# Optimization experiments

Measured on AMD Instinct MI355X. Metric: run time of the kernel, lower is better.

Reference implementation:

```python
import jax, jax.numpy as jnp
import numpy as np

X = 512; Y = 512; C = 3; NK = 15
DT = 0.2; DD = 2; SIGMA = 0.95
THETA_X = 2.0; N_EXP = 2.0
K_SIZE = 16

# mesh-grid positions, cell centers at +0.5 (matches construct_mesh_grid)
POS = (jnp.stack(jnp.meshgrid(jnp.arange(X), jnp.arange(Y), indexing='ij'), axis=-1) + 0.5).astype(jnp.float32)  # [X,Y,2]


def _dwconv(img, k):
    # img [X,Y,C'] -> depthwise 3x3 cross-correlation with 'same' zero padding (matches torch conv2d)
    z = img.transpose(2, 0, 1)[None]                      # [1,C',X,Y]
    kern = jnp.tile(k[None, None], (z.shape[1], 1, 1, 1))  # [C',1,3,3]
    out = jax.lax.conv_general_dilated(z, kern, (1, 1), 'SAME', feature_group_count=z.shape[1])
    return out[0].transpose(1, 2, 0)


def _sobel(img):
    # returns [X,Y,2,C'] with (sy, sx) stacked on axis 2, matching torch code order
    kx = jnp.array([[-1., 0., 1.], [-2., 0., 2.], [-1., 0., 1.]], jnp.float32)
    return jnp.stack([_dwconv(img, kx.T), _dwconv(img, kx)], axis=2)


def _reintegrate(grid, F):
    # Flow-Lenia reintegration tracking: 25 static roll offsets, fused accumulation
    ma = DD - SIGMA
    mu = POS[..., None] + jnp.clip(DT * F, -ma, ma)  # [X,Y,2,C]
    mu = jnp.clip(mu, SIGMA, X - SIGMA)
    clip_hi = min(1.0, 2.0 * SIGMA)
    inv_area = 1.0 / (4.0 * SIGMA ** 2)
    acc = jnp.zeros_like(grid)
    for dx in range(-DD, DD + 1):
        for dy in range(-DD, DD + 1):
            gridR = jnp.roll(grid, (dx, dy), (0, 1))
            muR = jnp.roll(mu, (dx, dy), (0, 1))
            sz = 0.5 - jnp.abs(POS[..., None] - muR) + SIGMA
            area = jnp.prod(jnp.clip(sz, 0.0, clip_hi), axis=2) * inv_area  # [X,Y,C]
            acc = acc + gridR * area
    return acc


def _forward(x, Ks, m, s, h, w_c1, c0):
    # spectral kernels: normalize, fftshift, fft2 (matches construct_kernels)
    Ksn = Ks / Ks.sum(axis=(0, 1), keepdims=True)
    fk = jnp.fft.fft2(jnp.fft.fftshift(Ksn, axes=(0, 1)), axes=(0, 1))  # [X,Y,NK] complex
    fXs = jnp.fft.fft2(x, axes=(0, 1))
    Us = jnp.fft.ifft2(fk * fXs[:, :, c0], axes=(0, 1)).real            # [X,Y,NK]
    # growth * h (note: h appears again inside w_c1, faithful to original double multiply)
    Gs = (jnp.exp(-(((Us - m) / s) ** 2) * 0.5) * 2.0 - 1.0) * h
    Hs = jnp.einsum('xyk,kc->xyc', Gs, w_c1)                             # [X,Y,C]
    grad_u = _sobel(Hs)                                                  # [X,Y,2,C]
    grad_x = _sobel(x.sum(-1, keepdims=True))                            # [X,Y,2,1]
    alpha = jnp.clip((x[:, :, None, :] / THETA_X) ** N_EXP, 0.0, 1.0)    # [X,Y,1,C]
    F = grad_u * (1.0 - alpha) - grad_x * alpha                          # [X,Y,2,C]
    return _reintegrate(x, F)


def setup_inputs() -> dict:
    key = jax.random.key(0)
    k1, k2, k3, k4, k5 = jax.random.split(key, 5)
    x = jax.random.uniform(k1, (X, Y, C), jnp.float32)
    # ring kernels per construct_kernels (non-sparse branch)
    mg = np.mgrid[-X // 2:X // 2, -Y // 2:Y // 2]
    base = np.linalg.norm(mg, axis=0).astype(np.float32)
    ks_list = []
    for i in range(NK):
        r = 0.6 + 0.04 * i
        D = base / ((K_SIZE + 15) * r)
        sig = 0.5 * (np.tanh(-(D - 1.0) * 10.0 / 2.0) + 1.0)
        bell = np.exp(-(D - 0.5) ** 2 / 0.15)
        ks_list.append(sig * bell)
    Ks = jnp.asarray(np.stack(ks_list, -1).astype(np.float32))
    m = 0.1 + 0.3 * jax.random.uniform(k2, (NK,), jnp.float32)
    s = 0.03 + 0.15 * jax.random.uniform(k3, (NK,), jnp.float32)
    h = 0.3 + 0.7 * jax.random.uniform(k4, (NK,), jnp.float32)
    c0 = jax.random.randint(k5, (NK,), 0, C, jnp.int32)
    c1 = jnp.arange(NK) % C
    w_c1 = jax.nn.one_hot(c1, C, dtype=jnp.float32) * h[:, None]
    return {"x": x, "Ks": Ks, "m": m, "s": s, "h": h, "w_c1": w_c1, "c0": c0}


def reference(x, Ks, m, s, h, w_c1, c0):
    return _forward(x, Ks, m, s, h, w_c1, c0)
```

## Files before the change

### kernel.cpp

```cpp
#include <hip/hip_runtime.h>
#include <math.h>

#define NPIX 262144
#define NKER 15
#define PI_F 3.14159265358979323846f
#define HW 264
#define HWR 264
#define CS 578
#define SK(n) ((n) + ((n) >> 3))

__device__ __forceinline__ float2 cadd(float2 a, float2 b) { return make_float2(a.x + b.x, a.y + b.y); }
__device__ __forceinline__ float2 csub(float2 a, float2 b) { return make_float2(a.x - b.x, a.y - b.y); }
__device__ __forceinline__ float2 cmul(float2 a, float2 b) {
  return make_float2(a.x * b.x - a.y * b.y, a.x * b.y + a.y * b.x);
}
__device__ __forceinline__ float2 cmulc(float2 a, float2 b) {
  return make_float2(a.x * b.x + a.y * b.y, a.y * b.x - a.x * b.y);
}

__device__ __forceinline__ void build_tw(int lane, float2* pA, float2* pB) {
  float s, c;
  sincosf(-2.0f * PI_F * (float)lane / 512.0f, &s, &c);
  float2 w1 = make_float2(c, s);
  int h = lane & ~7;
  float2 wh = make_float2(__shfl(c, h, 64), __shfl(s, h, 64));
  pA[0] = w1;
  pA[1] = cmul(w1, w1);
  pA[2] = cmul(pA[1], w1);
  pA[3] = cmul(pA[1], pA[1]);
  pA[4] = cmul(pA[3], w1);
  pA[5] = cmul(pA[3], pA[1]);
  pA[6] = cmul(pA[3], pA[2]);
  pB[0] = wh;
  pB[1] = cmul(wh, wh);
  pB[2] = cmul(pB[1], wh);
  pB[3] = cmul(pB[1], pB[1]);
  pB[4] = cmul(pB[3], wh);
  pB[5] = cmul(pB[3], pB[1]);
  pB[6] = cmul(pB[3], pB[2]);
}

template <bool INV>
__device__ __forceinline__ void dft8(float2 a[8]) {
  const float R = 0.70710678118654752f;
  float2 t0 = cadd(a[0], a[4]), u0 = csub(a[0], a[4]);
  float2 t1 = cadd(a[1], a[5]), u1 = csub(a[1], a[5]);
  float2 t2 = cadd(a[2], a[6]), u2 = csub(a[2], a[6]);
  float2 t3 = cadd(a[3], a[7]), u3 = csub(a[3], a[7]);
  u1 = INV ? make_float2(R * (u1.x - u1.y), R * (u1.x + u1.y))
           : make_float2(R * (u1.x + u1.y), R * (u1.y - u1.x));
  u2 = INV ? make_float2(-u2.y, u2.x) : make_float2(u2.y, -u2.x);
  u3 = INV ? make_float2(-R * (u3.x + u3.y), R * (u3.x - u3.y))
           : make_float2(R * (u3.y - u3.x), -R * (u3.x + u3.y));
  float2 e0 = cadd(t0, t2), f0 = csub(t0, t2);
  float2 e1 = cadd(t1, t3), f1 = csub(t1, t3);
  f1 = INV ? make_float2(-f1.y, f1.x) : make_float2(f1.y, -f1.x);
  float2 g0 = cadd(u0, u2), h0 = csub(u0, u2);
  float2 g1 = cadd(u1, u3), h1 = csub(u1, u3);
  h1 = INV ? make_float2(-h1.y, h1.x) : make_float2(h1.y, -h1.x);
  a[0] = cadd(e0, e1); a[4] = csub(e0, e1);
  a[2] = cadd(f0, f1); a[6] = csub(f0, f1);
  a[1] = cadd(g0, g1); a[5] = csub(g0, g1);
  a[3] = cadd(h0, h1); a[7] = csub(h0, h1);
}

template <bool INV>
__device__ __forceinline__ void fft512_r8(float2 a[8], float2* buf, int lane,
                                          const float2* pA, const float2* pB) {
  dft8<INV>(a);
#pragma unroll
  for (int q = 1; q < 8; ++q) a[q] = INV ? cmulc(a[q], pA[q - 1]) : cmul(a[q], pA[q - 1]);
#pragma unroll
  for (int q = 0; q < 8; ++q) buf[9 * lane + q] = a[q];
#pragma unroll
  for (int q = 0; q < 8; ++q) a[q] = buf[SK(lane + 64 * q)];
  dft8<INV>(a);
#pragma unroll
  for (int q = 1; q < 8; ++q) a[q] = INV ? cmulc(a[q], pB[q - 1]) : cmul(a[q], pB[q - 1]);
  int h = lane & ~7;
  int b2 = 9 * h + (lane - h);
#pragma unroll
  for (int q = 0; q < 8; ++q) buf[b2 + 9 * q] = a[q];
#pragma unroll
  for (int q = 0; q < 8; ++q) a[q] = buf[SK(lane + 64 * q)];
  dft8<INV>(a);
}

__device__ __forceinline__ void split_store_halfplane(float2 a[8], float2* buf, int lane,
                                                      float2* d0, float2* d1) {
#pragma unroll
  for (int q = 0; q < 8; ++q) buf[SK(lane + 64 * q)] = a[q];
#pragma unroll
  for (int q = 0; q < 4; ++q) {
    int v = lane + 64 * q;
    int mir = (512 - v) & 511;
    float2 P = a[q];
    float2 Qc = buf[SK(mir)];
    float2 Q = make_float2(Qc.x, -Qc.y);
    d0[v] = make_float2(0.5f * (P.x + Q.x), 0.5f * (P.y + Q.y));
    d1[v] = make_float2(0.5f * (P.y - Q.y), -0.5f * (P.x - Q.x));
  }
  if (lane == 0) {
    float2 P = a[4];
    d0[256] = make_float2(P.x, 0.f);
    d1[256] = make_float2(P.y, 0.f);
  }
}

__global__ __launch_bounds__(512, 4) void rows_all(
    const float* __restrict__ Ks, const float* __restrict__ x,
    float* __restrict__ partial, float* __restrict__ AkR,
    float2* __restrict__ AxH) {
  __shared__ float krow[512 * NKER];
  __shared__ float2 scr[8][CS];
  __shared__ float psum[480];
  int t = threadIdx.x, wave = t >> 6, lane = t & 63;
  float2 pA[7], pB[7];
  build_tw(lane, pA, pB);
  if (blockIdx.x < 512) {
    int b = blockIdx.x;
    int rs = (b + 256) & 511;
    const float2* src = (const float2*)Ks + (size_t)rs * 3840;
    float2* kr2 = (float2*)krow;
    for (int i = t; i < 3840; i += 512) kr2[i] = src[i];
    __syncthreads();
    if (t < 480) {
      int k = t >> 5, yg = t & 31;
      float s = 0.f;
      int base = yg * 16;
#pragma unroll
      for (int y = 0; y < 16; ++y) s += krow[(base + y) * NKER + k];
      psum[t] = s;
    }
    {
      int k1 = 2 * wave, k2 = k1 + 1;
      float2 a[8];
      bool nz = false;
#pragma unroll
      for (int q = 0; q < 8; ++q) {
        int ys = (lane + 64 * q + 256) & 511;
        float re = krow[ys * NKER + k1];
        float im = (k2 < NKER) ? krow[ys * NKER + k2] : 0.f;
        a[q] = make_float2(re, im);
        nz |= (re != 0.f) || (im != 0.f);
      }
      float* d0 = AkR + ((size_t)k1 * 512 + b) * HWR;
      float* d1 = AkR + ((size_t)k2 * 512 + b) * HWR;
      if (__any((int)nz)) {
        fft512_r8<false>(a, &scr[wave][0], lane, pA, pB);
#pragma unroll
        for (int q = 0; q < 4; ++q) {
          int v = lane + 64 * q;
          d0[v] = a[q].x; d1[v] = a[q].y;
        }
        if (lane == 0) { d0[256] = a[4].x; d1[256] = a[4].y; }
      } else {
#pragma unroll
        for (int q = 0; q < 4; ++q) {
          int v = lane + 64 * q;
          d0[v] = 0.f; d1[v] = 0.f;
        }
        if (lane == 0) { d0[256] = 0.f; d1[256] = 0.f; }
      }
    }
    __syncthreads();
    if (t < NKER) {
      float s = 0.f;
#pragma unroll
      for (int g = 0; g < 32; ++g) s += psum[(t << 5) + g];
      partial[b * 16 + t] = s;
    }
  } else {
    int job = (blockIdx.x - 512) * 8 + wave;
    int c = job >> 8;
    int rp = job & 255;
    int r0 = rp, r1 = rp + 256;
    float2 a[8];
#pragma unroll
    for (int q = 0; q < 8; ++q) {
      int y = lane + 64 * q;
      a[q] = make_float2(x[((size_t)r0 * 512 + y) * 3 + c],
                         x[((size_t)r1 * 512 + y) * 3 + c]);
    }
    fft512_r8<false>(a, &scr[wave][0], lane, pA, pB);
    float2* d0 = AxH + ((size_t)c * 512 + r0) * HW;
    float2* d1 = AxH + ((size_t)c * 512 + r1) * HW;
    split_store_halfplane(a, &scr[wave][0], lane, d0, d1);
  }
}

__global__ __launch_bounds__(512, 4) void xkcols(
    const float2* __restrict__ AxH, const float* __restrict__ AkR,
    float2* __restrict__ FxT, float* __restrict__ FkT,
    const float* __restrict__ partial, float* __restrict__ sums) {
  __shared__ float2 buf[8 * CS];
  __shared__ float red[512];
  int t = threadIdx.x;
  if (blockIdx.x == 33) {
    if (blockIdx.y != 0) return;
    int k = t & 15, g = t >> 4;
    float acc = 0.f;
    for (int b = g; b < 512; b += 32) acc += partial[b * 16 + k];
    red[t] = acc;
    __syncthreads();
    if (t < 16) {
      float s = 0.f;
#pragma unroll
      for (int g2 = 0; g2 < 32; ++g2) s += red[g2 * 16 + t];
      sums[t] = s;
    }
    return;
  }
  int c = t >> 6, lane = t & 63;
  int col0 = blockIdx.x << 3;
  float2 pA[7], pB[7];
  build_tw(lane, pA, pB);
  if (blockIdx.y < 3) {
    int ch = blockIdx.y;
    const float2* bx = AxH + (size_t)ch * 512 * HW;
#pragma unroll
    for (int u = 0; u < 8; ++u) {
      int idx = (u << 9) + t;
      int row = idx >> 3, cc = idx & 7;
      buf[cc * CS + SK(row)] = bx[(size_t)row * HW + col0 + cc];
    }
    __syncthreads();
    float2 a[8];
#pragma unroll
    for (int q = 0; q < 8; ++q) a[q] = buf[c * CS + SK(lane + 64 * q)];
    fft512_r8<false>(a, &buf[c * CS], lane, pA, pB);
    float2* dst = FxT + ((size_t)ch * HW + col0 + c) * 512;
#pragma unroll
    for (int q = 0; q < 8; ++q) dst[lane + 64 * q] = a[q];
  } else {
    int pr = blockIdx.y - 3;
    int k1 = 2 * pr, k2 = k1 + 1;
    const float* s1 = AkR + (size_t)k1 * 512 * HWR;
    const float* s2 = AkR + (size_t)k2 * 512 * HWR;
#pragma unroll
    for (int u = 0; u < 8; ++u) {
      int idx = (u << 9) + t;
      int row = idx >> 3, cc = idx & 7;
      buf[cc * CS + row] = make_float2(s1[(size_t)row * HWR + col0 + cc],
                                       s2[(size_t)row * HWR + col0 + cc]);
    }
    __syncthreads();
    float2 a[8];
#pragma unroll
    for (int q = 0; q < 8; ++q) a[q] = buf[c * CS + lane + 64 * q];
    fft512_r8<false>(a, &buf[c * CS], lane, pA, pB);
    float* e1 = FkT + ((size_t)k1 * HWR + col0 + c) * 512;
    float* e2 = FkT + ((size_t)k2 * HWR + col0 + c) * 512;
#pragma unroll
    for (int q = 0; q < 8; ++q) {
      int v = lane + 64 * q;
      e1[v] = a[q].x;
      e2[v] = a[q].y;
    }
  }
}

__global__ __launch_bounds__(512, 4) void fused_cols(
    float2* __restrict__ AkH, const float* __restrict__ FkT,
    const float2* __restrict__ FxT, const int* __restrict__ c0) {
  __shared__ float2 buf[8 * CS];
  int t = threadIdx.x;
  int col0 = blockIdx.x << 3, k = blockIdx.y;
  int c = t >> 6, lane = t & 63;
  float2 pA[7], pB[7];
  build_tw(lane, pA, pB);
  const float* fk = FkT + ((size_t)k * HWR + col0 + c) * 512;
  const float2* fx = FxT + ((size_t)c0[k] * HW + col0 + c) * 512;
  float2 a[8];
#pragma unroll
  for (int q = 0; q < 8; ++q) {
    int v = lane + 64 * q;
    float s = fk[v];
    float2 xv = fx[v];
    a[q] = make_float2(s * xv.x, s * xv.y);
  }
  fft512_r8<true>(a, &buf[c * CS], lane, pA, pB);
#pragma unroll
  for (int q = 0; q < 8; ++q) buf[c * CS + SK(lane + 64 * q)] = a[q];
  __syncthreads();
  float2* bk = AkH + (size_t)k * 512 * HW;
#pragma unroll
  for (int u = 0; u < 8; ++u) {
    int idx = (u << 9) + t;
    int row = idx >> 3, cc = idx & 7;
    bk[(size_t)row * HW + col0 + cc] = buf[cc * CS + SK(row)];
  }
}

__global__ __launch_bounds__(512, 4) void irows_growth_combine(
    const float2* __restrict__ AkH, const float* __restrict__ sums,
    const float* __restrict__ m, const float* __restrict__ s,
    const float* __restrict__ h, const float* __restrict__ w,
    float* __restrict__ Hs) {
  __shared__ float2 scr[8][CS];
  __shared__ float accL[4][3][512];
  __shared__ float mk[16], isk[16], hk[16], wk[16][3], sck[16];
  int t = threadIdx.x, wave = t >> 6, lane = t & 63;
  int row = blockIdx.x;
  if (t < NKER) {
    mk[t] = m[t]; isk[t] = 1.0f / s[t]; hk[t] = h[t];
    sck[t] = 1.0f / (sums[t] * 262144.0f);
    wk[t][0] = w[t * 3 + 0]; wk[t][1] = w[t * 3 + 1]; wk[t][2] = w[t * 3 + 2];
  }
  __syncthreads();
  float2 pA[7], pB[7];
  build_tw(lane, pA, pB);
  float acc[3][8];
#pragma unroll
  for (int cc = 0; cc < 3; ++cc)
#pragma unroll
    for (int q = 0; q < 8; ++q) acc[cc][q] = 0.f;
  {
    int slot = wave;
    int k1 = 2 * slot, k2 = 2 * slot + 1;
    bool dual = (k2 < NKER);
    const float2* p1 = AkH + ((size_t)k1 * 512 + row) * HW;
    const float2* p2 = AkH + ((size_t)(dual ? k2 : k1) * 512 + row) * HW;
    float2 a[8];
#pragma unroll
    for (int q = 0; q < 8; ++q) {
      int v = lane + 64 * q;
      if (v <= 256) {
        float2 A1 = p1[v];
        float2 A2 = dual ? p2[v] : make_float2(0.f, 0.f);
        a[q] = make_float2(A1.x - A2.y, A1.y + A2.x);
      } else {
        int mi = 512 - v;
        float2 A1 = p1[mi];
        float2 A2 = dual ? p2[mi] : make_float2(0.f, 0.f);
        a[q] = make_float2(A1.x + A2.y, -A1.y + A2.x);
      }
    }
    fft512_r8<true>(a, &scr[wave][0], lane, pA, pB);
    float m1 = mk[k1], i1 = isk[k1], h1 = hk[k1], s1 = sck[k1];
    float w10 = wk[k1][0], w11 = wk[k1][1], w12 = wk[k1][2];
#pragma unroll
    for (int q = 0; q < 8; ++q) {
      float tt = (a[q].x * s1 - m1) * i1;
      float g = (expf(-0.5f * tt * tt) * 2.0f - 1.0f) * h1;
      acc[0][q] += g * w10; acc[1][q] += g * w11; acc[2][q] += g * w12;
    }
    if (dual) {
      float m2 = mk[k2], i2 = isk[k2], h2 = hk[k2], s2 = sck[k2];
      float w20 = wk[k2][0], w21 = wk[k2][1], w22 = wk[k2][2];
#pragma unroll
      for (int q = 0; q < 8; ++q) {
        float tt = (a[q].y * s2 - m2) * i2;
        float g = (expf(-0.5f * tt * tt) * 2.0f - 1.0f) * h2;
        acc[0][q] += g * w20; acc[1][q] += g * w21; acc[2][q] += g * w22;
      }
    }
  }
  if (wave < 4) {
#pragma unroll
    for (int cc = 0; cc < 3; ++cc)
#pragma unroll
      for (int q = 0; q < 8; ++q) accL[wave][cc][lane + 64 * q] = acc[cc][q];
  }
  __syncthreads();
  if (wave >= 4) {
#pragma unroll
    for (int cc = 0; cc < 3; ++cc)
#pragma unroll
      for (int q = 0; q < 8; ++q) accL[wave - 4][cc][lane + 64 * q] += acc[cc][q];
  }
  __syncthreads();
#pragma unroll
  for (int cc = 0; cc < 3; ++cc) {
    float v = accL[0][cc][t] + accL[1][cc][t] + accL[2][cc][t] + accL[3][cc][t];
    Hs[(size_t)cc * NPIX + (size_t)row * 512 + t] = v;
  }
}

__global__ void flow_reint(const float* __restrict__ x, const float* __restrict__ Hs,
                           float* __restrict__ out) {
  __shared__ float tS[7][496];
  __shared__ float muT[400 * 6];
  int ox = (blockIdx.x >> 5) << 4;
  int oy = (blockIdx.x & 31) << 4;
  for (int i = threadIdx.x; i < 484; i += 256) {
    int li = i / 22, lj = i % 22;
    int qx = (ox - 3 + li) & 511, qy = (oy - 3 + lj) & 511;
    int q = (qx << 9) | qy;
    float h0 = Hs[q], h1 = Hs[NPIX + q], h2 = Hs[2 * NPIX + q];
    float x0 = x[(size_t)q * 3 + 0], x1 = x[(size_t)q * 3 + 1], x2 = x[(size_t)q * 3 + 2];
    tS[0][i] = h0; tS[1][i] = h1; tS[2][i] = h2;
    tS[3][i] = x0 + x1 + x2;
    tS[4][i] = x0; tS[5][i] = x1; tS[6][i] = x2;
  }
  __syncthreads();
  for (int i = threadIdx.x; i < 400; i += 256) {
    int hi = i / 20, hj = i % 20;
    int qx = (ox - 2 + hi) & 511, qy = (oy - 2 + hj) & 511;
    float syH0 = 0.f, syH1 = 0.f, syH2 = 0.f;
    float sxH0 = 0.f, sxH1 = 0.f, sxH2 = 0.f;
    float syX = 0.f, sxX = 0.f;
#pragma unroll
    for (int di = -1; di <= 1; ++di) {
#pragma unroll
      for (int dj = -1; dj <= 1; ++dj) {
        if (di == 0 && dj == 0) continue;
        int xi = qx + di, yj = qy + dj;
        if ((unsigned)xi >= 512u || (unsigned)yj >= 512u) continue;
        int l = (hi + 1 + di) * 22 + (hj + 1 + dj);
        float wy = (float)di * ((dj == 0) ? 2.f : 1.f);
        float wx = (float)dj * ((di == 0) ? 2.f : 1.f);
        float h0 = tS[0][l], h1 = tS[1][l], h2 = tS[2][l];
        syH0 += wy * h0; syH1 += wy * h1; syH2 += wy * h2;
        sxH0 += wx * h0; sxH1 += wx * h1; sxH2 += wx * h2;
        float xs = tS[3][l];
        syX += wy * xs; sxX += wx * xs;
      }
    }
    int lc = (hi + 1) * 22 + (hj + 1);
    float cxq = (float)qx + 0.5f, cyq = (float)qy + 0.5f;
    float syH[3] = {syH0, syH1, syH2};
    float sxH[3] = {sxH0, sxH1, sxH2};
    int b6 = i * 6;
#pragma unroll
    for (int c = 0; c < 3; ++c) {
      float xc = tS[4 + c][lc];
      float tt = xc * 0.5f;
      float alpha = fminf(tt * tt, 1.0f);
      float F0 = syH[c] * (1.f - alpha) - syX * alpha;
      float F1 = sxH[c] * (1.f - alpha) - sxX * alpha;
      float m0 = cxq + fminf(fmaxf(0.2f * F0, -1.05f), 1.05f);
      float m1 = cyq + fminf(fmaxf(0.2f * F1, -1.05f), 1.05f);
      muT[b6 + c]     = fminf(fmaxf(m0, 0.95f), 511.05f);
      muT[b6 + 3 + c] = fminf(fmaxf(m1, 0.95f), 511.05f);
    }
  }
  __syncthreads();
  int o = threadIdx.x;
  int lx = o >> 4, ly = o & 15;
  int px_ = ox + lx, py_ = oy + ly;
  float cx = (float)px_ + 0.5f, cy = (float)py_ + 0.5f;
  float a0 = 0.f, a1 = 0.f, a2 = 0.f;
#pragma unroll
  for (int dx = -2; dx <= 2; ++dx) {
    int hi = lx + 2 - dx;
#pragma unroll
    for (int dy = -2; dy <= 2; ++dy) {
      int hj = ly + 2 - dy;
      int b6 = (hi * 20 + hj) * 6;
      int lb = (hi + 1) * 22 + (hj + 1);
      float wv;
      wv = fminf(fmaxf(1.45f - fabsf(cx - muT[b6 + 0]), 0.f), 1.f) *
           fminf(fmaxf(1.45f - fabsf(cy - muT[b6 + 3]), 0.f), 1.f);
      a0 += tS[4][lb] * wv;
      wv = fminf(fmaxf(1.45f - fabsf(cx - muT[b6 + 1]), 0.f), 1.f) *
           fminf(fmaxf(1.45f - fabsf(cy - muT[b6 + 4]), 0.f), 1.f);
      a1 += tS[5][lb] * wv;
      wv = fminf(fmaxf(1.45f - fabsf(cx - muT[b6 + 2]), 0.f), 1.f) *
           fminf(fmaxf(1.45f - fabsf(cy - muT[b6 + 5]), 0.f), 1.f);
      a2 += tS[6][lb] * wv;
    }
  }
  const float inv_area = 0.27700831f;
  size_t p = (size_t)((px_ << 9) | py_);
  out[p * 3 + 0] = a0 * inv_area;
  out[p * 3 + 1] = a1 * inv_area;
  out[p * 3 + 2] = a2 * inv_area;
}

extern "C" void kernel_launch(void* const* d_in, const int* in_sizes, int n_in,
                              void* d_out, int out_size, void* d_ws, size_t ws_size,
                              hipStream_t stream) {
  const float* x    = (const float*)d_in[0];
  const float* Ks   = (const float*)d_in[1];
  const float* m    = (const float*)d_in[2];
  const float* s    = (const float*)d_in[3];
  const float* h    = (const float*)d_in[4];
  const float* w_c1 = (const float*)d_in[5];
  const int*   c0   = (const int*)d_in[6];
  float* out = (float*)d_out;

  char* ws = (char*)d_ws;
  size_t off = 0;
  float* sums    = (float*)(ws + off); off += 1024;
  float* partial = (float*)(ws + off); off += 512 * 16 * 4;
  float2* AxH  = (float2*)(ws + off); off += (size_t)3 * 512 * HW * 8;
  float2* AkH  = (float2*)(ws + off); off += (size_t)16 * 512 * HW * 8;
  float2* FxT  = (float2*)(ws + off); off += (size_t)3 * HW * 512 * 8;
  float*  AkR  = (float*)(ws + off);  off += (size_t)16 * 512 * HWR * 4;
  float*  FkT  = (float*)(ws + off);  off += (size_t)16 * HWR * 512 * 4;
  float*  Hs   = (float*)(ws + off);  off += (size_t)3 * NPIX * 4;

  rows_all<<<608, 512, 0, stream>>>(Ks, x, partial, AkR, AxH);
  xkcols<<<dim3(34, 11), 512, 0, stream>>>(AxH, AkR, FxT, FkT, partial, sums);
  fused_cols<<<dim3(33, NKER), 512, 0, stream>>>(AkH, FkT, FxT, c0);
  irows_growth_combine<<<512, 512, 0, stream>>>(AkH, sums, m, s, h, w_c1, Hs);
  flow_reint<<<1024, 256, 0, stream>>>(x, Hs, out);
}
```

Before: 126.5 us.

## Fuse kernel column FFT into spectral multiply and inverse column FFT

The forward column FFT of the kernel spectra moves out of the x-column kernel and into the fused multiply/inverse-column kernel, which now handles a pair of kernels per block. Each kernel spectrum is consumed in registers straight after its transform, so the FkT intermediate buffer and its global round trip go away. In exchange the fused kernel gets fewer blocks (8 pairs instead of 15 kernels) with more serial work each, while the x-column kernel launches fewer blocks and can no longer run the kernel-spectrum FFTs alongside the x FFTs.

```diff
diff --git a/kernel.cpp b/kernel.cpp
--- a/kernel.cpp
+++ b/kernel.cpp
@@ -189,9 +189,8 @@
   }
 }
 
-__global__ __launch_bounds__(512, 4) void xkcols(
-    const float2* __restrict__ AxH, const float* __restrict__ AkR,
-    float2* __restrict__ FxT, float* __restrict__ FkT,
+__global__ __launch_bounds__(512, 4) void xcols(
+    const float2* __restrict__ AxH, float2* __restrict__ FxT,
     const float* __restrict__ partial, float* __restrict__ sums) {
   __shared__ float2 buf[8 * CS];
   __shared__ float red[512];
@@ -212,83 +211,93 @@
     return;
   }
   int c = t >> 6, lane = t & 63;
-  int col0 = blockIdx.x << 3;
+  int col0 = blockIdx.x << 3, ch = blockIdx.y;
   float2 pA[7], pB[7];
   build_tw(lane, pA, pB);
-  if (blockIdx.y < 3) {
-    int ch = blockIdx.y;
-    const float2* bx = AxH + (size_t)ch * 512 * HW;
+  const float2* bx = AxH + (size_t)ch * 512 * HW;
+#pragma unroll
+  for (int u = 0; u < 8; ++u) {
+    int idx = (u << 9) + t;
+    int row = idx >> 3, cc = idx & 7;
+    buf[cc * CS + SK(row)] = bx[(size_t)row * HW + col0 + cc];
+  }
+  __syncthreads();
+  float2 a[8];
+#pragma unroll
+  for (int q = 0; q < 8; ++q) a[q] = buf[c * CS + SK(lane + 64 * q)];
+  fft512_r8<false>(a, &buf[c * CS], lane, pA, pB);
+  float2* dst = FxT + ((size_t)ch * HW + col0 + c) * 512;
+#pragma unroll
+  for (int q = 0; q < 8; ++q) dst[lane + 64 * q] = a[q];
+}
+
+__global__ __launch_bounds__(512, 4) void fused_cols_pair(
+    float2* __restrict__ AkH, const float* __restrict__ AkR,
+    const float2* __restrict__ FxT, const int* __restrict__ c0) {
+  __shared__ float2 buf[8 * CS];
+  int t = threadIdx.x, wave = t >> 6, lane = t & 63;
+  int col0 = blockIdx.x << 3;
+  int pr = blockIdx.y;
+  int k1 = 2 * pr, k2 = k1 + 1;
+  bool dual = (k2 < NKER);
+  float2 pA[7], pB[7];
+  build_tw(lane, pA, pB);
+  const float* s1 = AkR + (size_t)k1 * 512 * HWR;
+  const float* s2 = AkR + (size_t)(dual ? k2 : k1) * 512 * HWR;
+#pragma unroll
+  for (int u = 0; u < 8; ++u) {
+    int idx = (u << 9) + t;
+    int row = idx >> 3, cc = idx & 7;
+    buf[cc * CS + SK(row)] = make_float2(s1[(size_t)row * HWR + col0 + cc],
+                                         s2[(size_t)row * HWR + col0 + cc]);
+  }
+  __syncthreads();
+  float2 z[8];
+#pragma unroll
+  for (int q = 0; q < 8; ++q) z[q] = buf[wave * CS + SK(lane + 64 * q)];
+  fft512_r8<false>(z, &buf[wave * CS], lane, pA, pB);
+  {
+    const float2* fx = FxT + ((size_t)c0[k1] * HW + col0 + wave) * 512;
+    float2 a[8];
+#pragma unroll
+    for (int q = 0; q < 8; ++q) {
+      float s = z[q].x;
+      float2 xv = fx[lane + 64 * q];
+      a[q] = make_float2(s * xv.x, s * xv.y);
+    }
+    fft512_r8<true>(a, &buf[wave * CS], lane, pA, pB);
+#pragma unroll
+    for (int q = 0; q < 8; ++q) buf[wave * CS + SK(lane + 64 * q)] = a[q];
+    __syncthreads();
+    float2* bk = AkH + (size_t)k1 * 512 * HW;
 #pragma unroll
     for (int u = 0; u < 8; ++u) {
       int idx = (u << 9) + t;
       int row = idx >> 3, cc = idx & 7;
-      buf[cc * CS + SK(row)] = bx[(size_t)row * HW + col0 + cc];
-    }
+      bk[(size_t)row * HW + col0 + cc] = buf[cc * CS + SK(row)];
+    }
+  }
+  if (dual) {
     __syncthreads();
+    const float2* fx = FxT + ((size_t)c0[k2] * HW + col0 + wave) * 512;
     float2 a[8];
 #pragma unroll
-    for (int q = 0; q < 8; ++q) a[q] = buf[c * CS + SK(lane + 64 * q)];
-    fft512_r8<false>(a, &buf[c * CS], lane, pA, pB);
-    float2* dst = FxT + ((size_t)ch * HW + col0 + c) * 512;
-#pragma unroll
-    for (int q = 0; q < 8; ++q) dst[lane + 64 * q] = a[q];
-  } else {
-    int pr = blockIdx.y - 3;
-    int k1 = 2 * pr, k2 = k1 + 1;
-    const float* s1 = AkR + (size_t)k1 * 512 * HWR;
-    const float* s2 = AkR + (size_t)k2 * 512 * HWR;
+    for (int q = 0; q < 8; ++q) {
+      float s = z[q].y;
+      float2 xv = fx[lane + 64 * q];
+      a[q] = make_float2(s * xv.x, s * xv.y);
+    }
+    fft512_r8<true>(a, &buf[wave * CS], lane, pA, pB);
+#pragma unroll
+    for (int q = 0; q < 8; ++q) buf[wave * CS + SK(lane + 64 * q)] = a[q];
+    __syncthreads();
+    float2* bk = AkH + (size_t)k2 * 512 * HW;
 #pragma unroll
     for (int u = 0; u < 8; ++u) {
       int idx = (u << 9) + t;
       int row = idx >> 3, cc = idx & 7;
-      buf[cc * CS + row] = make_float2(s1[(size_t)row * HWR + col0 + cc],
-                                       s2[(size_t)row * HWR + col0 + cc]);
-    }
-    __syncthreads();
-    float2 a[8];
-#pragma unroll
-    for (int q = 0; q < 8; ++q) a[q] = buf[c * CS + lane + 64 * q];
-    fft512_r8<false>(a, &buf[c * CS], lane, pA, pB);
-    float* e1 = FkT + ((size_t)k1 * HWR + col0 + c) * 512;
-    float* e2 = FkT + ((size_t)k2 * HWR + col0 + c) * 512;
-#pragma unroll
-    for (int q = 0; q < 8; ++q) {
-      int v = lane + 64 * q;
-      e1[v] = a[q].x;
-      e2[v] = a[q].y;
-    }
-  }
-}
-
-__global__ __launch_bounds__(512, 4) void fused_cols(
-    float2* __restrict__ AkH, const float* __restrict__ FkT,
-    const float2* __restrict__ FxT, const int* __restrict__ c0) {
-  __shared__ float2 buf[8 * CS];
-  int t = threadIdx.x;
-  int col0 = blockIdx.x << 3, k = blockIdx.y;
-  int c = t >> 6, lane = t & 63;
-  float2 pA[7], pB[7];
-  build_tw(lane, pA, pB);
-  const float* fk = FkT + ((size_t)k * HWR + col0 + c) * 512;
-  const float2* fx = FxT + ((size_t)c0[k] * HW + col0 + c) * 512;
-  float2 a[8];
-#pragma unroll
-  for (int q = 0; q < 8; ++q) {
-    int v = lane + 64 * q;
-    float s = fk[v];
-    float2 xv = fx[v];
-    a[q] = make_float2(s * xv.x, s * xv.y);
-  }
-  fft512_r8<true>(a, &buf[c * CS], lane, pA, pB);
-#pragma unroll
-  for (int q = 0; q < 8; ++q) buf[c * CS + SK(lane + 64 * q)] = a[q];
-  __syncthreads();
-  float2* bk = AkH + (size_t)k * 512 * HW;
-#pragma unroll
-  for (int u = 0; u < 8; ++u) {
-    int idx = (u << 9) + t;
-    int row = idx >> 3, cc = idx & 7;
-    bk[(size_t)row * HW + col0 + cc] = buf[cc * CS + SK(row)];
+      bk[(size_t)row * HW + col0 + cc] = buf[cc * CS + SK(row)];
+    }
   }
 }
 
@@ -488,12 +497,11 @@
   float2* AkH  = (float2*)(ws + off); off += (size_t)16 * 512 * HW * 8;
   float2* FxT  = (float2*)(ws + off); off += (size_t)3 * HW * 512 * 8;
   float*  AkR  = (float*)(ws + off);  off += (size_t)16 * 512 * HWR * 4;
-  float*  FkT  = (float*)(ws + off);  off += (size_t)16 * HWR * 512 * 4;
   float*  Hs   = (float*)(ws + off);  off += (size_t)3 * NPIX * 4;
 
   rows_all<<<608, 512, 0, stream>>>(Ks, x, partial, AkR, AxH);
-  xkcols<<<dim3(34, 11), 512, 0, stream>>>(AxH, AkR, FxT, FkT, partial, sums);
-  fused_cols<<<dim3(33, NKER), 512, 0, stream>>>(AkH, FkT, FxT, c0);
+  xcols<<<dim3(34, 3), 512, 0, stream>>>(AxH, FxT, partial, sums);
+  fused_cols_pair<<<dim3(33, 8), 512, 0, stream>>>(AkH, AkR, FxT, c0);
   irows_growth_combine<<<512, 512, 0, stream>>>(AkH, sums, m, s, h, w_c1, Hs);
   flow_reint<<<1024, 256, 0, stream>>>(x, Hs, out);
 }
```

After: 132.8 us. 1.05x slower.
